# Performance work log

Hardware: AMD Instinct MI355X
Metric: run time of the kernel (lower is better)

The kernel has to match this reference:

```python
import jax, jax.numpy as jnp
import numpy as np

N = 80         # max_num_nodes
ITERS = 50     # mpm max_iters


def setup_inputs() -> dict:
    key = jax.random.key(0)
    k1, k2 = jax.random.split(key)
    # reconstructed (predicted) adjacency probabilities, kept strictly in (0,1) for BCE
    recon = jax.random.uniform(k1, (N, N), jnp.float32) * 0.98 + 0.01
    # ground-truth binary adjacency, symmetric with self-loops (adj[i,i] used in S build)
    adj = (jax.random.uniform(k2, (N, N), jnp.float32) > 0.5).astype(jnp.float32)
    adj = jnp.maximum(adj, adj.T)
    adj = adj.at[jnp.arange(N), jnp.arange(N)].set(1.0)
    return {"recon_grf": recon, "original_grf": adj}


def _forward(recon, adj):
    # degree-like matching features
    out_features = jnp.sum(recon, axis=1)   # recon node features g_a
    adj_features = jnp.sum(adj, axis=1)     # original node features f_i

    adj_d = jnp.diagonal(adj)               # adj[i,i]
    rec_d = jnp.diagonal(recon)             # recon[a,a]
    eye = jnp.eye(N, dtype=recon.dtype)
    off = 1.0 - eye

    # off-diagonal edge affinities (zero when i==j or a==b, matching the loop skips)
    src = adj * adj_d[:, None] * adj_d[None, :] * off     # [i,j] = adj[i,j]*adj[i,i]*adj[j,j]
    tgt = recon * rec_d[:, None] * rec_d[None, :] * off   # [a,b] = recon[a,b]*recon[a,a]*recon[b,b]

    # diagonal affinities S[i,i,a,a] = adj[i,i]*recon[a,a]*sim(f_i, g_a)
    sim = 1.0 / (jnp.abs(adj_features[:, None] - out_features[None, :]) + 1.0)  # [i,a]
    d = adj_d[:, None] * rec_d[None, :] * sim                                   # [i,a]

    # full affinity tensor S[i,j,a,b]  (N^4 elements)
    S = src[:, :, None, None] * tgt[None, None, :, :] \
        + (eye[:, :, None, None] * eye[None, None, :, :]) * d[:, None, :, None]

    # max-pooling matching (mpm), 50 iterations; checkpoint keeps vjp memory at 1 iter
    @jax.checkpoint
    def step(x):
        # pooled[i,j,a] = max_b x[j,b] * S[i,j,a,b]
        pooled = jnp.max(x[None, :, None, :] * S, axis=3)     # [i,j,a]
        neigh = jnp.sum(pooled * off[:, :, None], axis=1)     # sum over j != i -> [i,a]
        x_new = x * d + neigh                                 # d[i,a] == S[i,i,a,a]
        return x_new / jnp.linalg.norm(x_new)

    x0 = jnp.full((N, N), 1.0 / N, dtype=recon.dtype)
    assignment, _ = jax.lax.scan(lambda x, _: (step(x), None), x0, None, length=ITERS)

    # BCE on the upper triangle (incl. diagonal), mean reduction like F.binary_cross_entropy
    iu = jnp.triu_indices(N)
    t = adj[iu]
    p = recon[iu]
    loss = -jnp.mean(t * jnp.log(p) + (1.0 - t) * jnp.log(1.0 - p))
    return loss, assignment


def reference(recon_grf, original_grf):
    return _forward(recon_grf, original_grf)
```

## Files before the change

### kernel.cpp

```cpp
#include <hip/hip_runtime.h>
#include <math.h>

#define NN 80
#define MITERS 50
#define NTHREADS 1024

typedef _Float16 h8 __attribute__((ext_vector_type(8)));
typedef float f4 __attribute__((ext_vector_type(4)));

__device__ __forceinline__ unsigned pk_mul_f16(unsigned a, unsigned b) {
  unsigned d; asm("v_pk_mul_f16 %0, %1, %2" : "=v"(d) : "v"(a), "v"(b)); return d;
}
__device__ __forceinline__ unsigned pk_max_f16(unsigned a, unsigned b) {
  unsigned d; asm("v_pk_max_f16 %0, %1, %2" : "=v"(d) : "v"(a), "v"(b)); return d;
}
__device__ __forceinline__ h8 as_h8(uint4 u) {
  union { uint4 u; h8 h; } x; x.u = u; return x.h;
}

#define OFF_XH    0
#define OFF_TT    13120
#define OFF_MM    26240
#define OFF_SRCH  92800
#define OFF_DLT   109440
#define OFF_FR    136320
#define OFF_FA    136640
#define OFF_RD    136960
#define OFF_AD    137280
#define OFF_WSUM  137600
#define OFF_LSUM  137728
#define LDS_BYTES 137792

#define PB(r, k) ((((r) >> 2) * 656) + (((k) >> 1) * 16) + (((r) & 3) * 4) + (((k) & 1) * 2))


#define DO_TILE(I0, A0, XO)                                                   \
  {                                                                           \
    f4 acc = {0.f, 0.f, 0.f, 0.f};                                            \
    _Pragma("unroll")                                                         \
    for (int ks = 0; ks < 3; ++ks) {                                          \
      const uint4 afr =                                                       \
          *(const uint4*)(SRCHb + ((I0) + la) * 208 + ks * 64 + gr * 16);     \
      const int blk = (ks * 4 + gr) ^ mkey;                                   \
      const int mo = ((A0) + la) * 208 + blk * 16;                            \
      const uint4 b0 = *(const uint4*)(MMb + mo);                             \
      const uint4 b1 = *(const uint4*)(MMb + 16640 + mo);                     \
      const uint4 b2 = *(const uint4*)(MMb + 33280 + mo);                     \
      const uint4 b3 = *(const uint4*)(MMb + 49920 + mo);                     \
      uint4 bb;                                                               \
      bb.x = pk_max_f16(pk_max_f16(b0.x, b1.x), pk_max_f16(b2.x, b3.x));      \
      bb.y = pk_max_f16(pk_max_f16(b0.y, b1.y), pk_max_f16(b2.y, b3.y));      \
      bb.z = pk_max_f16(pk_max_f16(b0.z, b1.z), pk_max_f16(b2.z, b3.z));      \
      bb.w = pk_max_f16(pk_max_f16(b0.w, b1.w), pk_max_f16(b2.w, b3.w));      \
      acc = __builtin_amdgcn_mfma_f32_16x16x32_f16(as_h8(afr),                \
                                                   as_h8(bb), acc, 0, 0, 0);  \
    }                                                                         \
    const int col = (A0) + la;                                                \
    const int rb = (I0) + gr * 4;                                             \
    const float4 dl = *(const float4*)(DLTb + col * 336 + rb * 4);            \
    const float n0 = fmaf(XO[0], dl.x, acc[0]) * inv;                         \
    const float n1 = fmaf(XO[1], dl.y, acc[1]) * inv;                         \
    const float n2 = fmaf(XO[2], dl.z, acc[2]) * inv;                         \
    const float n3 = fmaf(XO[3], dl.w, acc[3]) * inv;                         \
    ss += n0 * n0 + n1 * n1 + n2 * n2 + n3 * n3;                              \
    XO[0] = n0; XO[1] = n1; XO[2] = n2; XO[3] = n3;                           \
    char* xa = XHb + (((I0) >> 2) + gr) * 656 + (col >> 1) * 16 + (col & 1) * 2; \
    *(_Float16*)(xa) = (_Float16)n0;                                          \
    *(_Float16*)(xa + 4) = (_Float16)n1;                                      \
    *(_Float16*)(xa + 8) = (_Float16)n2;                                      \
    *(_Float16*)(xa + 12) = (_Float16)n3;                                     \
  }

__global__ void __launch_bounds__(NTHREADS, 4)
__attribute__((amdgpu_waves_per_eu(4, 4)))
grf_kernel(const float* __restrict__ recon, const float* __restrict__ adj,
           float* __restrict__ out) {
  extern __shared__ char ldsb[];
  char* XHb = ldsb + OFF_XH;
  char* TTb = ldsb + OFF_TT;
  char* MMb = ldsb + OFF_MM;
  char* SRCHb = ldsb + OFF_SRCH;
  char* DLTb = ldsb + OFF_DLT;
  float* FR = (float*)(ldsb + OFF_FR);
  float* FA = (float*)(ldsb + OFF_FA);
  float* RD = (float*)(ldsb + OFF_RD);
  float* AD = (float*)(ldsb + OFF_AD);
  float* WSUM = (float*)(ldsb + OFF_WSUM);
  float* LSUM = (float*)(ldsb + OFF_LSUM);

  const int t = threadIdx.x;
  const int wave = t >> 6, lane = t & 63;
  const int la = lane & 15, gr = lane >> 4;
  const int mkey = (la >> 2) & 3;

  if (t < 80) {
    float s = 0.f;
    for (int b = 0; b < NN; ++b) s += recon[t * NN + b];
    FR[t] = s;
    RD[t] = recon[t * NN + t];
  } else if (t < 160) {
    const int i = t - 80;
    float s = 0.f;
    for (int j = 0; j < NN; ++j) s += adj[i * NN + j];
    FA[i] = s;
    AD[i] = adj[i * NN + i];
  }
  if (t < 32) {
    const float q = (float)(_Float16)(1.0f / 80.0f);
    WSUM[t] = (t == 0) ? 6400.0f * q * q : 0.f;
  }
  __syncthreads();

  float lacc = 0.f;
  for (int f = t; f < NN * NN; f += NTHREADS) {
    const int r = f / NN, c = f - (f / NN) * NN;
    *(_Float16*)(XHb + PB(r, c)) = (_Float16)(1.0f / 80.0f);
    const float tv = (r == c) ? 0.f : recon[r * NN + c] * RD[r] * RD[c];
    *(_Float16*)(TTb + PB(r, c)) = (_Float16)tv;
    *(float*)(DLTb + (c * 84 + r) * 4) =
        AD[r] * RD[c] / (fabsf(FA[r] - FR[c]) + 1.f);
    const float sv = (r == c) ? 0.f : adj[r * NN + c] * AD[r] * AD[c];
    *(_Float16*)(SRCHb + (r * 104 + c) * 2) = (_Float16)sv;
    if (c >= r) {
      const float tb = adj[f], p = recon[f];
      lacc -= tb * logf(p) + (1.f - tb) * logf(1.f - p);
    }
  }
  for (int f = t; f < 1920; f += NTHREADS) {
    const int r = f / 24, j = 80 + (f - (f / 24) * 24);
    *(_Float16*)(SRCHb + (r * 104 + j) * 2) = (_Float16)0.f;
  }
  for (int f = t; f < 16640; f += NTHREADS) *(unsigned*)(MMb + f * 4) = 0u;

  #pragma unroll
  for (int off = 32; off > 0; off >>= 1) lacc += __shfl_down(lacc, off, 64);
  if (lane == 0) LSUM[wave] = lacc;
  __syncthreads();
  if (t == 0) {
    float s = 0.f;
    for (int w = 0; w < 16; ++w) s += LSUM[w];
    out[0] = s / 3240.f;
  }

  const int i00 = (wave / 5) * 16, a00 = (wave % 5) * 16;
  const int tt1 = wave + 16;
  const bool has2 = tt1 < 25;
  const int i01 = has2 ? (tt1 / 5) * 16 : 0;
  const int a01 = has2 ? (tt1 % 5) * 16 : 0;

  const int g = t >> 8;
  const int u = t & 255;
  const bool actA = (u < 200);
  const int rtA = u / 20;
  const int ctA = u - rtA * 20;
  const char* xbase = XHb + (2 * rtA) * 656 + g * 160;
  char* mwp = MMb + g * 16640 + (ctA * 4) * 208 + ((rtA ^ (ctA & 3)) * 16);

  uint4 tr[10];
  #pragma unroll
  for (int cc = 0; cc < 10; ++cc)
    tr[cc] = *(const uint4*)(TTb + ctA * 656 + (g * 10 + cc) * 16);

  float xo0[4], xo1[4];
  #pragma unroll
  for (int k = 0; k < 4; ++k) xo0[k] = xo1[k] = (float)(_Float16)(1.0f / 80.0f);

  for (int it = 0; it < MITERS; ++it) {
    if (actA) {
      unsigned m[8][4];
      #pragma unroll
      for (int r = 0; r < 8; ++r)
        #pragma unroll
        for (int c = 0; c < 4; ++c) m[r][c] = 0u;
      #pragma unroll
      for (int cc = 0; cc < 10; ++cc) {
        const uint4 x0 = *(const uint4*)(xbase + cc * 16);
        const uint4 x1 = *(const uint4*)(xbase + 656 + cc * 16);
        const unsigned xr[8] = {x0.x, x0.y, x0.z, x0.w, x1.x, x1.y, x1.z, x1.w};
        const unsigned tc[4] = {tr[cc].x, tr[cc].y, tr[cc].z, tr[cc].w};
        #pragma unroll
        for (int r = 0; r < 8; ++r)
          #pragma unroll
          for (int c = 0; c < 4; ++c)
            m[r][c] = pk_max_f16(m[r][c], pk_mul_f16(xr[r], tc[c]));
      }
      #pragma unroll
      for (int c = 0; c < 4; ++c) {
        unsigned lo[8];
        #pragma unroll
        for (int r = 0; r < 8; ++r) {
          const unsigned v = m[r][c];
          lo[r] = pk_max_f16(v, (v >> 16) | (v << 16)) & 0xffffu;
        }
        const uint4 w = make_uint4(lo[0] | (lo[1] << 16), lo[2] | (lo[3] << 16),
                                   lo[4] | (lo[5] << 16), lo[6] | (lo[7] << 16));
        *(uint4*)(mwp + c * 208) = w;
      }
    }
    __syncthreads();

    const float* WIN = WSUM + ((it & 1) << 4);
    const float4 wa = *(const float4*)(WIN);
    const float4 wb = *(const float4*)(WIN + 4);
    const float4 wc = *(const float4*)(WIN + 8);
    const float4 wd = *(const float4*)(WIN + 12);
    const float tot = ((wa.x + wa.y) + (wa.z + wa.w)) +
                      ((wb.x + wb.y) + (wb.z + wb.w)) +
                      ((wc.x + wc.y) + (wc.z + wc.w)) +
                      ((wd.x + wd.y) + (wd.z + wd.w));
    const float inv = 1.0f / sqrtf(tot);

    float ss = 0.f;
    DO_TILE(i00, a00, xo0);
    if (has2) DO_TILE(i01, a01, xo1);

    #pragma unroll
    for (int off = 32; off > 0; off >>= 1) ss += __shfl_down(ss, off, 64);
    if (lane == 0) WSUM[(((it + 1) & 1) << 4) + wave] = ss;
    __syncthreads();
  }

  {
    const float* WF = WSUM + ((MITERS & 1) << 4);
    float tot = 0.f;
    #pragma unroll
    for (int w = 0; w < 16; ++w) tot += WF[w];
    const float finv = 1.0f / sqrtf(tot);
    for (int f = t; f < NN * NN; f += NTHREADS) {
      const int i = f / NN, a = f - (f / NN) * NN;
      out[1 + f] = (float)*(const _Float16*)(XHb + PB(i, a)) * finv;
    }
  }
}

extern "C" void kernel_launch(void* const* d_in, const int* in_sizes, int n_in,
                              void* d_out, int out_size, void* d_ws, size_t ws_size,
                              hipStream_t stream) {
  const float* recon = (const float*)d_in[0];
  const float* adj   = (const float*)d_in[1];
  float* out = (float*)d_out;
  (void)in_sizes; (void)n_in; (void)out_size; (void)d_ws; (void)ws_size;

  hipFuncSetAttribute(reinterpret_cast<const void*>(grf_kernel),
                      hipFuncAttributeMaxDynamicSharedMemorySize, LDS_BYTES);
  grf_kernel<<<1, NTHREADS, LDS_BYTES, stream>>>(recon, adj, out);
}
```

Measured before the change: 404.5 us.

## Split max-pool over 2 b-groups with 4x4 tiles instead of 4 groups with 8x4

The pooled max stage now splits the b dimension into 2 groups of 40 instead of 4 groups of 20. Each thread computes a 4-row by 4-col register tile over 20 chunks and reads T from LDS each chunk instead of caching it in registers. This halves the partial-max buffer and LDS footprint, and the MFMA stage reads and reduces 2 partials instead of 4. The waves_per_eu attribute is dropped. In exchange each thread does more LDS reads per iteration, and register pressure changes.

```diff
diff --git a/kernel.cpp b/kernel.cpp
--- a/kernel.cpp
+++ b/kernel.cpp
@@ -21,15 +21,15 @@
 #define OFF_XH    0
 #define OFF_TT    13120
 #define OFF_MM    26240
-#define OFF_SRCH  92800
-#define OFF_DLT   109440
-#define OFF_FR    136320
-#define OFF_FA    136640
-#define OFF_RD    136960
-#define OFF_AD    137280
-#define OFF_WSUM  137600
-#define OFF_LSUM  137728
-#define LDS_BYTES 137792
+#define OFF_SRCH  59520
+#define OFF_DLT   76160
+#define OFF_FR    103040
+#define OFF_FA    103360
+#define OFF_RD    103680
+#define OFF_AD    104000
+#define OFF_WSUM  104320
+#define OFF_LSUM  104448
+#define LDS_BYTES 104512
 
 #define PB(r, k) ((((r) >> 2) * 656) + (((k) >> 1) * 16) + (((r) & 3) * 4) + (((k) & 1) * 2))
 
@@ -45,13 +45,11 @@
       const int mo = ((A0) + la) * 208 + blk * 16;                            \
       const uint4 b0 = *(const uint4*)(MMb + mo);                             \
       const uint4 b1 = *(const uint4*)(MMb + 16640 + mo);                     \
-      const uint4 b2 = *(const uint4*)(MMb + 33280 + mo);                     \
-      const uint4 b3 = *(const uint4*)(MMb + 49920 + mo);                     \
       uint4 bb;                                                               \
-      bb.x = pk_max_f16(pk_max_f16(b0.x, b1.x), pk_max_f16(b2.x, b3.x));      \
-      bb.y = pk_max_f16(pk_max_f16(b0.y, b1.y), pk_max_f16(b2.y, b3.y));      \
-      bb.z = pk_max_f16(pk_max_f16(b0.z, b1.z), pk_max_f16(b2.z, b3.z));      \
-      bb.w = pk_max_f16(pk_max_f16(b0.w, b1.w), pk_max_f16(b2.w, b3.w));      \
+      bb.x = pk_max_f16(b0.x, b1.x);                                          \
+      bb.y = pk_max_f16(b0.y, b1.y);                                          \
+      bb.z = pk_max_f16(b0.z, b1.z);                                          \
+      bb.w = pk_max_f16(b0.w, b1.w);                                          \
       acc = __builtin_amdgcn_mfma_f32_16x16x32_f16(as_h8(afr),                \
                                                    as_h8(bb), acc, 0, 0, 0);  \
     }                                                                         \
@@ -72,7 +70,6 @@
   }
 
 __global__ void __launch_bounds__(NTHREADS, 4)
-__attribute__((amdgpu_waves_per_eu(4, 4)))
 grf_kernel(const float* __restrict__ recon, const float* __restrict__ adj,
            float* __restrict__ out) {
   extern __shared__ char ldsb[];
@@ -130,7 +127,7 @@
     const int r = f / 24, j = 80 + (f - (f / 24) * 24);
     *(_Float16*)(SRCHb + (r * 104 + j) * 2) = (_Float16)0.f;
   }
-  for (int f = t; f < 16640; f += NTHREADS) *(unsigned*)(MMb + f * 4) = 0u;
+  for (int f = t; f < 8320; f += NTHREADS) *(unsigned*)(MMb + f * 4) = 0u;
 
   #pragma unroll
   for (int off = 32; off > 0; off >>= 1) lacc += __shfl_down(lacc, off, 64);
@@ -148,18 +145,15 @@
   const int i01 = has2 ? (tt1 / 5) * 16 : 0;
   const int a01 = has2 ? (tt1 % 5) * 16 : 0;
 
-  const int g = t >> 8;
-  const int u = t & 255;
-  const bool actA = (u < 200);
-  const int rtA = u / 20;
-  const int ctA = u - rtA * 20;
-  const char* xbase = XHb + (2 * rtA) * 656 + g * 160;
-  char* mwp = MMb + g * 16640 + (ctA * 4) * 208 + ((rtA ^ (ctA & 3)) * 16);
-
-  uint4 tr[10];
-  #pragma unroll
-  for (int cc = 0; cc < 10; ++cc)
-    tr[cc] = *(const uint4*)(TTb + ctA * 656 + (g * 10 + cc) * 16);
+  const int g = t >> 9;
+  const int u = t & 511;
+  const bool actA = (u < 400);
+  const int rt = u / 20;
+  const int ct = u - rt * 20;
+  const char* xAp = XHb + rt * 656 + g * 320;
+  const char* tAp = TTb + ct * 656 + g * 320;
+  char* mwp = MMb + g * 16640 + (ct * 4) * 208 +
+              (((rt >> 1) ^ (ct & 3)) * 16) + ((rt & 1) * 8);
 
   float xo0[4], xo1[4];
   #pragma unroll
@@ -167,34 +161,33 @@
 
   for (int it = 0; it < MITERS; ++it) {
     if (actA) {
-      unsigned m[8][4];
+      unsigned m[4][4];
       #pragma unroll
-      for (int r = 0; r < 8; ++r)
+      for (int r = 0; r < 4; ++r)
         #pragma unroll
         for (int c = 0; c < 4; ++c) m[r][c] = 0u;
-      #pragma unroll
-      for (int cc = 0; cc < 10; ++cc) {
-        const uint4 x0 = *(const uint4*)(xbase + cc * 16);
-        const uint4 x1 = *(const uint4*)(xbase + 656 + cc * 16);
-        const unsigned xr[8] = {x0.x, x0.y, x0.z, x0.w, x1.x, x1.y, x1.z, x1.w};
-        const unsigned tc[4] = {tr[cc].x, tr[cc].y, tr[cc].z, tr[cc].w};
+      #pragma unroll 4
+      for (int cc = 0; cc < 20; ++cc) {
+        const uint4 xq = *(const uint4*)(xAp + cc * 16);
+        const uint4 tq = *(const uint4*)(tAp + cc * 16);
+        const unsigned xr[4] = {xq.x, xq.y, xq.z, xq.w};
+        const unsigned tc[4] = {tq.x, tq.y, tq.z, tq.w};
         #pragma unroll
-        for (int r = 0; r < 8; ++r)
+        for (int r = 0; r < 4; ++r)
           #pragma unroll
           for (int c = 0; c < 4; ++c)
             m[r][c] = pk_max_f16(m[r][c], pk_mul_f16(xr[r], tc[c]));
       }
       #pragma unroll
       for (int c = 0; c < 4; ++c) {
-        unsigned lo[8];
+        unsigned lo[4];
         #pragma unroll
-        for (int r = 0; r < 8; ++r) {
+        for (int r = 0; r < 4; ++r) {
           const unsigned v = m[r][c];
           lo[r] = pk_max_f16(v, (v >> 16) | (v << 16)) & 0xffffu;
         }
-        const uint4 w = make_uint4(lo[0] | (lo[1] << 16), lo[2] | (lo[3] << 16),
-                                   lo[4] | (lo[5] << 16), lo[6] | (lo[7] << 16));
-        *(uint4*)(mwp + c * 208) = w;
+        const uint2 w = make_uint2(lo[0] | (lo[1] << 16), lo[2] | (lo[3] << 16));
+        *(uint2*)(mwp + c * 208) = w;
       }
     }
     __syncthreads();
```

Measured after the change: 368.4 us. 8.9% less time.
